# Optimization experiments

Hardware: AMD Instinct MI355X
Metric: run time of the kernel (lower is better)

Reference implementation:

```python
import jax, jax.numpy as jnp
import numpy as np

THRESH = 0.5
ALPHA = 0.5


def setup_inputs() -> dict:
    key = jax.random.key(0)
    k1, k2 = jax.random.split(key)
    B, N, C = 128, 43264, 5
    # BCELoss requires probabilities strictly inside (0,1); bound away from edges.
    x = jax.random.uniform(k1, (B, N, C), dtype=jnp.float32, minval=0.01, maxval=0.99)
    y = jax.random.uniform(k2, (B, N, C), dtype=jnp.float32, minval=0.01, maxval=0.99)
    return {"x": x, "y": y}


def reference(x, y):
    # Vectorized equivalent of the per-cell Python loop:
    # select cells where label confidence > thresh, then mean-reduce losses
    # over the selected set (torch MSELoss/BCELoss use mean reduction).
    m = (y[:, :, 0] > THRESH).astype(x.dtype)          # [B, N] selection mask
    face_num = jnp.sum(m)                              # number of selected cells
    scale = 1.0 + 1.0 / face_num

    # MSE over the 4 box coords of selected cells (mean over face_num*4 elems)
    se = jnp.square(x[:, :, 1:5] - y[:, :, 1:5])       # [B, N, 4]
    diff_box = scale * jnp.sum(se * m[:, :, None]) / (face_num * 4.0)

    # BCE over confidence of selected cells (mean over face_num elems)
    p = x[:, :, 0]                                     # predicted confidence [B, N]
    t = y[:, :, 0]                                     # target confidence   [B, N]
    bce = -(t * jnp.log(p) + (1.0 - t) * jnp.log1p(-p))
    diff_c = scale * jnp.sum(bce * m) / face_num

    # Background BCE: all confidences vs zeros -> -log(1-p), mean over all cells
    diff_bg = ALPHA * jnp.mean(-jnp.log1p(-p))

    return diff_box + diff_c + diff_bg
```

## Files before the change

kernel.cpp:

```cpp
#include <hip/hip_runtime.h>

#define THRESH 0.5f
#define ALPHA 0.5f
#define BLOCK 256
#define MAXGRID 2048

__global__ void mloss_partial(const float* __restrict__ x,
                              const float* __restrict__ y,
                              float4* __restrict__ part,
                              int ngroups, int nrows) {
    float cnt = 0.f, s_se = 0.f, s_bce = 0.f, s_bg = 0.f;
    const int stride = gridDim.x * blockDim.x;
    const int tid = blockIdx.x * blockDim.x + threadIdx.x;

    auto row = [&](float p, float t, float d0, float d1, float d2, float d3) {
        float l1m = log1pf(-p);
        s_bg -= l1m;
        float m = (t > THRESH) ? 1.f : 0.f;
        cnt += m;
        float se = d0*d0 + d1*d1 + d2*d2 + d3*d3;
        s_se += m * se;
        float bce = -(t * logf(p) + (1.f - t) * l1m);
        s_bce += m * bce;
    };

    for (int g = tid; g < ngroups; g += stride) {
        const float4* xv = (const float4*)(x + (size_t)g * 20);
        const float4* yv = (const float4*)(y + (size_t)g * 20);
        float4 a0 = xv[0], a1 = xv[1], a2 = xv[2], a3 = xv[3], a4 = xv[4];
        float4 b0 = yv[0], b1 = yv[1], b2 = yv[2], b3 = yv[3], b4 = yv[4];

        row(a0.x, b0.x, a0.y-b0.y, a0.z-b0.z, a0.w-b0.w, a1.x-b1.x);
        row(a1.y, b1.y, a1.z-b1.z, a1.w-b1.w, a2.x-b2.x, a2.y-b2.y);
        row(a2.z, b2.z, a2.w-b2.w, a3.x-b3.x, a3.y-b3.y, a3.z-b3.z);
        row(a3.w, b3.w, a4.x-b4.x, a4.y-b4.y, a4.z-b4.z, a4.w-b4.w);
    }

    for (int r = ngroups * 4 + tid; r < nrows; r += stride) {
        const float* xr = x + (size_t)r * 5;
        const float* yr = y + (size_t)r * 5;
        row(xr[0], yr[0], xr[1]-yr[1], xr[2]-yr[2], xr[3]-yr[3], xr[4]-yr[4]);
    }

    #pragma unroll
    for (int off = 32; off > 0; off >>= 1) {
        cnt   += __shfl_down(cnt,   off);
        s_se  += __shfl_down(s_se,  off);
        s_bce += __shfl_down(s_bce, off);
        s_bg  += __shfl_down(s_bg,  off);
    }

    __shared__ float4 lds[BLOCK / 64];
    const int wid = threadIdx.x >> 6;
    if ((threadIdx.x & 63) == 0)
        lds[wid] = make_float4(cnt, s_se, s_bce, s_bg);
    __syncthreads();
    if (threadIdx.x == 0) {
        float4 a = lds[0];
        #pragma unroll
        for (int w = 1; w < BLOCK / 64; ++w) {
            a.x += lds[w].x; a.y += lds[w].y; a.z += lds[w].z; a.w += lds[w].w;
        }
        part[blockIdx.x] = a;
    }
}

__global__ void mloss_final(const float4* __restrict__ part, int nparts,
                            float* __restrict__ out, float inv_total) {
    float cnt = 0.f, s_se = 0.f, s_bce = 0.f, s_bg = 0.f;
    for (int i = threadIdx.x; i < nparts; i += BLOCK) {
        float4 v = part[i];
        cnt += v.x; s_se += v.y; s_bce += v.z; s_bg += v.w;
    }
    #pragma unroll
    for (int off = 32; off > 0; off >>= 1) {
        cnt   += __shfl_down(cnt,   off);
        s_se  += __shfl_down(s_se,  off);
        s_bce += __shfl_down(s_bce, off);
        s_bg  += __shfl_down(s_bg,  off);
    }
    __shared__ float4 lds[BLOCK / 64];
    const int wid = threadIdx.x >> 6;
    if ((threadIdx.x & 63) == 0)
        lds[wid] = make_float4(cnt, s_se, s_bce, s_bg);
    __syncthreads();
    if (threadIdx.x == 0) {
        float4 a = lds[0];
        #pragma unroll
        for (int w = 1; w < BLOCK / 64; ++w) {
            a.x += lds[w].x; a.y += lds[w].y; a.z += lds[w].z; a.w += lds[w].w;
        }
        float f = a.x;
        float scale = 1.f + 1.f / f;
        float diff_box = scale * a.y / (f * 4.f);
        float diff_c   = scale * a.z / f;
        float diff_bg  = ALPHA * a.w * inv_total;
        out[0] = diff_box + diff_c + diff_bg;
    }
}

extern "C" void kernel_launch(void* const* d_in, const int* in_sizes, int n_in,
                              void* d_out, int out_size, void* d_ws, size_t ws_size,
                              hipStream_t stream) {
    const float* x = (const float*)d_in[0];
    const float* y = (const float*)d_in[1];
    float* out  = (float*)d_out;
    float4* part = (float4*)d_ws;

    int total   = in_sizes[0];
    int nrows   = total / 5;
    int ngroups = nrows / 4;

    int grid = (ngroups + BLOCK - 1) / BLOCK;
    if (grid > MAXGRID) grid = MAXGRID;

    mloss_partial<<<grid, BLOCK, 0, stream>>>(x, y, part, ngroups, nrows);
    mloss_final<<<1, BLOCK, 0, stream>>>(part, grid, out, 1.0f / (float)nrows);
}
```

Baseline: 48.55 us.

## Use wave-coalesced float4 tiles with shuffle-based row mask propagation

```diff
diff --git a/kernel.cpp b/kernel.cpp
--- a/kernel.cpp
+++ b/kernel.cpp
@@ -3,43 +3,80 @@
 #define THRESH 0.5f
 #define ALPHA 0.5f
 #define BLOCK 256
-#define MAXGRID 2048
 
-__global__ void mloss_partial(const float* __restrict__ x,
+__global__ void mloss_partial(const float4* __restrict__ xv,
+                              const float4* __restrict__ yv,
+                              const float* __restrict__ x,
                               const float* __restrict__ y,
                               float4* __restrict__ part,
-                              int ngroups, int nrows) {
+                              int ntiles, int nrows) {
     float cnt = 0.f, s_se = 0.f, s_bce = 0.f, s_bg = 0.f;
-    const int stride = gridDim.x * blockDim.x;
-    const int tid = blockIdx.x * blockDim.x + threadIdx.x;
+    const int lane   = threadIdx.x & 63;
+    const int gwave  = (blockIdx.x * BLOCK + threadIdx.x) >> 6;
+    const int nwaves = (gridDim.x * BLOCK) >> 6;
 
-    auto row = [&](float p, float t, float d0, float d1, float d2, float d3) {
-        float l1m = log1pf(-p);
-        s_bg -= l1m;
-        float m = (t > THRESH) ? 1.f : 0.f;
-        cnt += m;
-        float se = d0*d0 + d1*d1 + d2*d2 + d3*d3;
-        s_se += m * se;
-        float bce = -(t * logf(p) + (1.f - t) * l1m);
-        s_bce += m * bce;
-    };
-
-    for (int g = tid; g < ngroups; g += stride) {
-        const float4* xv = (const float4*)(x + (size_t)g * 20);
-        const float4* yv = (const float4*)(y + (size_t)g * 20);
-        float4 a0 = xv[0], a1 = xv[1], a2 = xv[2], a3 = xv[3], a4 = xv[4];
-        float4 b0 = yv[0], b1 = yv[1], b2 = yv[2], b3 = yv[3], b4 = yv[4];
-
-        row(a0.x, b0.x, a0.y-b0.y, a0.z-b0.z, a0.w-b0.w, a1.x-b1.x);
-        row(a1.y, b1.y, a1.z-b1.z, a1.w-b1.w, a2.x-b2.x, a2.y-b2.y);
-        row(a2.z, b2.z, a2.w-b2.w, a3.x-b3.x, a3.y-b3.y, a3.z-b3.z);
-        row(a3.w, b3.w, a4.x-b4.x, a4.y-b4.y, a4.z-b4.z, a4.w-b4.w);
+    int p[5];
+    {
+        const int add[5] = {0, 4, 3, 2, 1};
+        int lm5 = lane % 5;
+        #pragma unroll
+        for (int k = 0; k < 5; ++k) {
+            int v = lm5 + add[k];
+            p[k] = (v >= 5) ? v - 5 : v;
+        }
     }
 
-    for (int r = ngroups * 4 + tid; r < nrows; r += stride) {
+    for (int tile = gwave; tile < ntiles; tile += nwaves) {
+        size_t f0 = (size_t)tile * 320 + lane;
+        float4 X[5], Y[5];
+        #pragma unroll
+        for (int k = 0; k < 5; ++k) {
+            X[k] = xv[f0 + 64 * k];
+            Y[k] = yv[f0 + 64 * k];
+        }
+
+        float carry = 0.f;
+        #pragma unroll
+        for (int k = 0; k < 5; ++k) {
+            const int pk = p[k];
+            const float4 Xk = X[k], Yk = Y[k];
+
+            float my_t = (pk == 0) ? Yk.x : (pk == 1) ? Yk.y : (pk == 2) ? Yk.z : Yk.w;
+            float my_p = (pk == 0) ? Xk.x : (pk == 1) ? Xk.y : (pk == 2) ? Xk.z : Xk.w;
+            float my_m = (my_t > THRESH) ? 1.f : 0.f;
+
+            float pm_up  = __shfl_up(my_m, 1);
+            float prev_m = (lane == 0) ? carry : pm_up;
+            carry = __shfl(my_m, 63);
+
+            float has = (pk < 4) ? 1.f : 0.f;
+            float l1m = __logf(1.f - my_p);
+            float lg  = __logf(my_p);
+            s_bg -= has * l1m;
+            float hm = has * my_m;
+            cnt += hm;
+            s_bce -= hm * (my_t * lg + (1.f - my_t) * l1m);
+
+            float d, w;
+            d = Xk.x - Yk.x; w = (pk == 0) ? 0.f : ((0 < pk) ? prev_m : my_m); s_se += w * d * d;
+            d = Xk.y - Yk.y; w = (pk == 1) ? 0.f : ((1 < pk) ? prev_m : my_m); s_se += w * d * d;
+            d = Xk.z - Yk.z; w = (pk == 2) ? 0.f : ((2 < pk) ? prev_m : my_m); s_se += w * d * d;
+            d = Xk.w - Yk.w; w = (pk == 3) ? 0.f : ((3 < pk) ? prev_m : my_m); s_se += w * d * d;
+        }
+    }
+
+    for (int r = ntiles * 256 + blockIdx.x * BLOCK + threadIdx.x; r < nrows;
+         r += gridDim.x * BLOCK) {
         const float* xr = x + (size_t)r * 5;
         const float* yr = y + (size_t)r * 5;
-        row(xr[0], yr[0], xr[1]-yr[1], xr[2]-yr[2], xr[3]-yr[3], xr[4]-yr[4]);
+        float pp = xr[0], tt = yr[0];
+        float m = (tt > THRESH) ? 1.f : 0.f;
+        float l1m = __logf(1.f - pp);
+        s_bg -= l1m;
+        cnt += m;
+        s_bce -= m * (tt * __logf(pp) + (1.f - tt) * l1m);
+        float d1 = xr[1]-yr[1], d2 = xr[2]-yr[2], d3 = xr[3]-yr[3], d4 = xr[4]-yr[4];
+        s_se += m * (d1*d1 + d2*d2 + d3*d3 + d4*d4);
     }
 
     #pragma unroll
@@ -104,16 +141,21 @@
                               hipStream_t stream) {
     const float* x = (const float*)d_in[0];
     const float* y = (const float*)d_in[1];
-    float* out  = (float*)d_out;
+    float* out   = (float*)d_out;
     float4* part = (float4*)d_ws;
 
-    int total   = in_sizes[0];
-    int nrows   = total / 5;
-    int ngroups = nrows / 4;
+    int total  = in_sizes[0];
+    int nrows  = total / 5;
+    int ntiles = total / 1280;
 
-    int grid = (ngroups + BLOCK - 1) / BLOCK;
-    if (grid > MAXGRID) grid = MAXGRID;
+    int waves_needed = (ntiles + 1) / 2;
+    int grid = (waves_needed + 3) / 4;
+    if (grid < 256) grid = 256;
+    if (grid > 4096) grid = 4096;
+    int wscap = (int)(ws_size / sizeof(float4));
+    if (grid > wscap) grid = wscap;
 
-    mloss_partial<<<grid, BLOCK, 0, stream>>>(x, y, part, ngroups, nrows);
+    mloss_partial<<<grid, BLOCK, 0, stream>>>((const float4*)x, (const float4*)y,
+                                              x, y, part, ntiles, nrows);
     mloss_final<<<1, BLOCK, 0, stream>>>(part, grid, out, 1.0f / (float)nrows);
 }
```

Result: faster. 41.91 us (-13.7%).
